# Optimization experiments

Hardware: AMD Instinct MI355X
Metric: run time of the kernel (lower is better)

The kernel has to match this reference:

```python
import jax, jax.numpy as jnp
import numpy as np

N_HEAD = 16


def setup_inputs() -> dict:
    key = jax.random.key(0)
    ks = jax.random.split(key, 6)
    B, S, D = 2, 2048, 1024
    w = 0.02
    return {
        "x": jax.random.normal(ks[0], (B, S, D), dtype=jnp.float32),
        "attention_mask": jnp.ones((B, S), dtype=jnp.int32),
        "Wq": jax.random.normal(ks[1], (D, D), dtype=jnp.float32) * w,
        "bq": jnp.zeros((D,), dtype=jnp.float32),
        "Wk": jax.random.normal(ks[2], (D, D), dtype=jnp.float32) * w,
        "bk": jnp.zeros((D,), dtype=jnp.float32),
        "Wv": jax.random.normal(ks[3], (D, D), dtype=jnp.float32) * w,
        "bv": jnp.zeros((D,), dtype=jnp.float32),
        "Wp": jax.random.normal(ks[4], (D, D), dtype=jnp.float32) * w,
        "bp": jnp.zeros((D,), dtype=jnp.float32),
    }


def reference(x, attention_mask, Wq, bq, Wk, bk, Wv, bv, Wp, bp):
    # x: (B,S,D); PyTorch Linear: y = x @ W.T + b
    B, S, D = x.shape
    H = N_HEAD
    HD = D // H
    scale = 1.0 / jnp.sqrt(jnp.asarray(HD, dtype=x.dtype))

    def heads(W, b):
        return (x @ W.T + b).reshape(B, S, H, HD).transpose(0, 2, 1, 3)  # (B,H,S,HD)

    q = heads(Wq, bq)
    k = heads(Wk, bk)
    v = heads(Wv, bv)

    logits = jnp.einsum("bhsd,bhtd->bhst", q, k) * scale  # (B,H,S,S)

    causal = jnp.tril(jnp.ones((S, S), dtype=bool))  # (S,S)
    am = attention_mask.astype(bool)
    mask = causal[None, None, :, :] & (am[:, None, :, None] & am[:, None, None, :])

    float_min = jnp.finfo(x.dtype).min
    logits = jnp.where(mask, logits, float_min)
    w = jax.nn.softmax(logits, axis=-1)  # dropout is identity in eval / p=0

    attn = jnp.einsum("bhst,bhtd->bhsd", w, v)  # (B,H,S,HD)
    attn = attn.transpose(0, 2, 1, 3).reshape(B, S, D)
    return attn @ Wp.T + bp
```

## Files before the change

### kernel.cpp

```cpp
#include <hip/hip_runtime.h>


#define BB 2
#define SS 2048
#define DD 1024
#define HH 16
#define HDD 64
#define NEG_BIG (-1.0e30f)
#define QSCL 0.18033688011112042f

typedef __attribute__((ext_vector_type(8))) short short8;
typedef __attribute__((ext_vector_type(4))) float floatx4;
typedef unsigned int u32;
#define AS_GLOBAL __attribute__((address_space(1)))
#define AS_LDS    __attribute__((address_space(3)))

__device__ __forceinline__ ushort f2bf(float f) {
    unsigned u = __float_as_uint(f);
    u += 0x7fffu + ((u >> 16) & 1u);
    return (ushort)(u >> 16);
}
__device__ __forceinline__ unsigned pk2(float a, float b) {
    return ((unsigned)f2bf(b) << 16) | (unsigned)f2bf(a);
}
__device__ __forceinline__ unsigned cvtpk(float a, float b) {
    unsigned r;
    asm("v_cvt_pk_bf16_f32 %0, %1, %2" : "=v"(r) : "v"(a), "v"(b));
    return r;
}
__device__ __forceinline__ void unpack8(const uint4 u, float* d) {
    d[0] = __uint_as_float(u.x << 16);
    d[1] = __uint_as_float(u.x & 0xffff0000u);
    d[2] = __uint_as_float(u.y << 16);
    d[3] = __uint_as_float(u.y & 0xffff0000u);
    d[4] = __uint_as_float(u.z << 16);
    d[5] = __uint_as_float(u.z & 0xffff0000u);
    d[6] = __uint_as_float(u.w << 16);
    d[7] = __uint_as_float(u.w & 0xffff0000u);
}
__device__ __forceinline__ void dma16(void* lds, const void* g) {
    __builtin_amdgcn_global_load_lds((const AS_GLOBAL u32*)g, (AS_LDS u32*)lds,
                                     16, 0, 0);
}

__global__ __launch_bounds__(256) void cvt_all(
    const float* __restrict__ x, const float* __restrict__ wq,
    const float* __restrict__ wk, const float* __restrict__ wv,
    const float* __restrict__ wp,
    ushort* __restrict__ dst, ushort* __restrict__ wp_dst)
{
    const size_t flat = ((size_t)blockIdx.x * 256 + threadIdx.x) * 8;
    const float* s;
    ushort* d = dst + flat;
    size_t off;
    float scl = 1.0f;
    if (flat < (size_t)4194304)      { s = x;  off = flat; }
    else if (flat < (size_t)5242880) { s = wq; off = flat - 4194304; scl = QSCL; }
    else if (flat < (size_t)6291456) { s = wk; off = flat - 5242880; }
    else if (flat < (size_t)7340032) { s = wv; off = flat - 6291456; }
    else { s = wp; off = flat - 7340032; d = wp_dst + off; }
    const float4 a = ((const float4*)(s + off))[0];
    const float4 b = ((const float4*)(s + off))[1];
    uint4 u;
    u.x = pk2(a.x * scl, a.y * scl); u.y = pk2(a.z * scl, a.w * scl);
    u.z = pk2(b.x * scl, b.y * scl); u.w = pk2(b.z * scl, b.w * scl);
    *(uint4*)d = u;
}

__global__ __launch_bounds__(256) void gemm_qkv_wa(
    const ushort* __restrict__ A,
    const ushort* __restrict__ W0, const ushort* __restrict__ W1,
    const ushort* __restrict__ W2,
    const float* __restrict__ B0, const float* __restrict__ B1,
    const float* __restrict__ B2,
    ushort* __restrict__ O0, ushort* __restrict__ O1, ushort* __restrict__ O2)
{
    __shared__ ushort As[128 * 32];
    __shared__ ushort Bs[128 * 32];
    __shared__ float bias_s[128];

    const int z = blockIdx.z;
    const ushort* W = (z == 0) ? W0 : (z == 1 ? W1 : W2);
    const float* bias = (z == 0) ? B0 : (z == 1 ? B1 : B2);
    ushort* out = (z == 0) ? O0 : (z == 1 ? O1 : O2);
    const bool isv = (z == 2);

    const int tid = threadIdx.x;
    const int bm = blockIdx.x * 128, bn = blockIdx.y * 128;
    const int wave = tid >> 6, lane = tid & 63, quad = lane >> 4, lm = lane & 15;
    const int r0 = tid >> 2, c0 = (tid & 3) * 8;

    if (tid < 128) {
        float bb = bias[bn + tid];
        if (z == 0) bb *= QSCL;
        bias_s[tid] = bb;
    }

    const floatx4 zz = {0.f, 0.f, 0.f, 0.f};
    floatx4 acc[16];
#pragma unroll
    for (int i = 0; i < 16; ++i) acc[i] = zz;

    for (int k0 = 0; k0 < DD; k0 += 32) {
        __syncthreads();
        dma16(&As[r0 * 32 + c0], A + (size_t)(bm + r0) * DD + k0 + c0);
        dma16(&As[(64 + r0) * 32 + c0], A + (size_t)(bm + 64 + r0) * DD + k0 + c0);
        dma16(&Bs[r0 * 32 + c0], W + (size_t)(bn + r0) * DD + k0 + c0);
        dma16(&Bs[(64 + r0) * 32 + c0], W + (size_t)(bn + 64 + r0) * DD + k0 + c0);
        __syncthreads();

        if (isv) {
            const short8 bf0 = *(const short8*)&Bs[(wave * 32 + lm) * 32 + quad * 8];
            const short8 bf1 = *(const short8*)&Bs[(wave * 32 + 16 + lm) * 32 + quad * 8];
#pragma unroll
            for (int i = 0; i < 8; ++i) {
                const short8 af = *(const short8*)&As[(i * 16 + lm) * 32 + quad * 8];
                acc[i * 2 + 0] = __builtin_amdgcn_mfma_f32_16x16x32_bf16(
                    af, bf0, acc[i * 2 + 0], 0, 0, 0);
                acc[i * 2 + 1] = __builtin_amdgcn_mfma_f32_16x16x32_bf16(
                    af, bf1, acc[i * 2 + 1], 0, 0, 0);
            }
        } else {
            const short8 af0 = *(const short8*)&As[(wave * 32 + lm) * 32 + quad * 8];
            const short8 af1 = *(const short8*)&As[(wave * 32 + 16 + lm) * 32 + quad * 8];
#pragma unroll
            for (int j = 0; j < 8; ++j) {
                const short8 bf = *(const short8*)&Bs[(j * 16 + lm) * 32 + quad * 8];
                acc[j] = __builtin_amdgcn_mfma_f32_16x16x32_bf16(
                    bf, af0, acc[j], 0, 0, 0);
                acc[8 + j] = __builtin_amdgcn_mfma_f32_16x16x32_bf16(
                    bf, af1, acc[8 + j], 0, 0, 0);
            }
        }
    }

    if (isv) {
        const int b = bm >> 11, sbase = bm & 2047;
#pragma unroll
        for (int j = 0; j < 2; ++j) {
            const int n = bn + wave * 32 + j * 16 + lm;
            const float bb = bias_s[n - bn];
            ushort* orow = out + ((size_t)(b * DD + n)) * SS;
#pragma unroll
            for (int i = 0; i < 8; ++i) {
                const floatx4 a = acc[i * 2 + j];
                ushort4 v;
                v.x = f2bf(a[0] + bb); v.y = f2bf(a[1] + bb);
                v.z = f2bf(a[2] + bb); v.w = f2bf(a[3] + bb);
                *(ushort4*)(orow + sbase + i * 16 + quad * 4) = v;
            }
        }
    } else {
#pragma unroll
        for (int i = 0; i < 2; ++i) {
            const int m = bm + wave * 32 + i * 16 + lm;
            const int b = m >> 11, s = m & 2047;
#pragma unroll
            for (int j = 0; j < 8; ++j) {
                const int nl = j * 16 + quad * 4;
                const int n = bn + nl;
                const int h = n >> 6, hd = n & 63;
                const floatx4 a = acc[i * 8 + j];
                ushort4 v;
                v.x = f2bf(a[0] + bias_s[nl + 0]);
                v.y = f2bf(a[1] + bias_s[nl + 1]);
                v.z = f2bf(a[2] + bias_s[nl + 2]);
                v.w = f2bf(a[3] + bias_s[nl + 3]);
                *(ushort4*)(out + (((size_t)(b * HH + h) * SS) + s) * HDD + hd) = v;
            }
        }
    }
}

__global__ __launch_bounds__(256) void gemm_proj_wa(
    const ushort* __restrict__ A, const ushort* __restrict__ W,
    const float* __restrict__ bias, float* __restrict__ out)
{
    __shared__ ushort As[64 * 32];
    __shared__ ushort Bs[128 * 32];
    __shared__ float bias_s[128];

    const int tid = threadIdx.x;
    const int bm = blockIdx.x * 64, bn = blockIdx.y * 128;
    const int wave = tid >> 6, lane = tid & 63, quad = lane >> 4, lm = lane & 15;
    const int r0 = tid >> 2, c0 = (tid & 3) * 8;

    if (tid < 128) bias_s[tid] = bias[bn + tid];

    const floatx4 zz = {0.f, 0.f, 0.f, 0.f};
    floatx4 acc[8];
#pragma unroll
    for (int j = 0; j < 8; ++j) acc[j] = zz;

    for (int k0 = 0; k0 < DD; k0 += 32) {
        __syncthreads();
        dma16(&As[r0 * 32 + c0], A + (size_t)(bm + (r0 & 63)) * DD + k0 + c0);
        dma16(&Bs[r0 * 32 + c0], W + (size_t)(bn + r0) * DD + k0 + c0);
        dma16(&Bs[(64 + r0) * 32 + c0], W + (size_t)(bn + 64 + r0) * DD + k0 + c0);
        __syncthreads();

        const short8 af = *(const short8*)&As[(wave * 16 + lm) * 32 + quad * 8];
#pragma unroll
        for (int j = 0; j < 8; ++j) {
            const short8 bf = *(const short8*)&Bs[(j * 16 + lm) * 32 + quad * 8];
            acc[j] = __builtin_amdgcn_mfma_f32_16x16x32_bf16(bf, af, acc[j], 0, 0, 0);
        }
    }

    const int m = bm + wave * 16 + lm;
#pragma unroll
    for (int j = 0; j < 8; ++j) {
        const int nl = j * 16 + quad * 4;
        float4 v;
        v.x = acc[j][0] + bias_s[nl + 0];
        v.y = acc[j][1] + bias_s[nl + 1];
        v.z = acc[j][2] + bias_s[nl + 2];
        v.w = acc[j][3] + bias_s[nl + 3];
        *(float4*)(out + (size_t)m * DD + bn + nl) = v;
    }
}

__global__ __launch_bounds__(256) void attn_mfma(
    const ushort* __restrict__ Q, const ushort* __restrict__ K,
    const ushort* __restrict__ Vt, const int* __restrict__ am,
    ushort* __restrict__ Opart, float* __restrict__ lbuf)
{
    __shared__ ushort Ks[64 * 72];
    __shared__ ushort Vts[64 * 72];
    __shared__ ushort Ps[4][32 * 72];
    __shared__ int amk_s[64];

    const int tid = threadIdx.x;
    const int wq = tid >> 6, lane = tid & 63, quad = lane >> 4, lm = lane & 15;
    const int bh = blockIdx.y, b = bh >> 4, h = bh & 15;
    const int qt = b ? (int)blockIdx.x : (int)(gridDim.x - 1 - blockIdx.x);
    const int split = blockIdx.z;
    const size_t base = (size_t)bh * SS * HDD;
    const size_t tbase = (size_t)bh * HDD * SS;
    const int* amrow = am + b * SS;
    const int q0 = qt * 128 + wq * 32;

    short8 qf[2][2];
#pragma unroll
    for (int sub = 0; sub < 2; ++sub) {
        const ushort* qp = Q + base + (size_t)(q0 + sub * 16 + lm) * HDD + quad * 8;
        qf[sub][0] = *(const short8*)qp;
        qf[sub][1] = *(const short8*)(qp + 32);
    }
    int amq[2];
#pragma unroll
    for (int sub = 0; sub < 2; ++sub) amq[sub] = amrow[q0 + sub * 16 + lm];
    const bool allq = __all(amq[0] != 0 && amq[1] != 0);

    const floatx4 zz = {0.f, 0.f, 0.f, 0.f};
    floatx4 o_acc[2][4];
#pragma unroll
    for (int sub = 0; sub < 2; ++sub)
#pragma unroll
        for (int n2 = 0; n2 < 4; ++n2) o_acc[sub][n2] = zz;
    float l_lane[2] = {0.f, 0.f};

    const int sr = tid >> 2, sc = (tid & 3) * 16;
    const int ktmax = 2 * qt + 1;

    uint4 kra, krb, vra, vrb;
    int amr = 1;
    {
        const ushort* kp = K + base + (size_t)(split * 64 + sr) * HDD + sc;
        kra = ((const uint4*)kp)[0]; krb = ((const uint4*)kp)[1];
        const ushort* vp = Vt + tbase + (size_t)sr * SS + split * 64 + sc;
        vra = ((const uint4*)vp)[0]; vrb = ((const uint4*)vp)[1];
        if (tid < 64) amr = amrow[split * 64 + tid];
    }
    *(uint4*)&Ks[sr * 72 + sc] = kra;
    *(uint4*)&Ks[sr * 72 + sc + 8] = krb;
    *(uint4*)&Vts[sr * 72 + sc] = vra;
    *(uint4*)&Vts[sr * 72 + sc + 8] = vrb;
    if (tid < 64) amk_s[tid] = amr;
    __syncthreads();

    for (int kt = split; kt <= ktmax; kt += 2) {
        const int nxt = kt + 2;
        const bool have_nxt = nxt <= ktmax;
        if (have_nxt) {
            const ushort* kp = K + base + (size_t)(nxt * 64 + sr) * HDD + sc;
            kra = ((const uint4*)kp)[0]; krb = ((const uint4*)kp)[1];
            const ushort* vp = Vt + tbase + (size_t)sr * SS + nxt * 64 + sc;
            vra = ((const uint4*)vp)[0]; vrb = ((const uint4*)vp)[1];
            if (tid < 64) amr = amrow[nxt * 64 + tid];
        }

        const bool allk = (__ballot(amk_s[lane] != 0) == ~0ull);
        const bool fast = allk & allq & ((kt * 64 + 63) <= q0);
        if (fast) {
#pragma unroll
            for (int nt = 0; nt < 4; ++nt) {
                const short8 kf0 = *(const short8*)&Ks[(nt * 16 + lm) * 72 + quad * 8];
                const short8 kf1 = *(const short8*)&Ks[(nt * 16 + lm) * 72 + 32 + quad * 8];
#pragma unroll
                for (int sub = 0; sub < 2; ++sub) {
                    floatx4 s = zz;
                    s = __builtin_amdgcn_mfma_f32_16x16x32_bf16(kf0, qf[sub][0], s, 0, 0, 0);
                    s = __builtin_amdgcn_mfma_f32_16x16x32_bf16(kf1, qf[sub][1], s, 0, 0, 0);
                    const float e0 = exp2f(fminf(s[0], 40.f));
                    const float e1 = exp2f(fminf(s[1], 40.f));
                    const float e2 = exp2f(fminf(s[2], 40.f));
                    const float e3 = exp2f(fminf(s[3], 40.f));
                    l_lane[sub] += (e0 + e1) + (e2 + e3);
                    uint2 pv;
                    pv.x = cvtpk(e0, e1); pv.y = cvtpk(e2, e3);
                    *(uint2*)&Ps[wq][(sub * 16 + lm) * 72 + nt * 16 + quad * 4] = pv;
                }
            }
        } else {
#pragma unroll
            for (int nt = 0; nt < 4; ++nt) {
                const short8 kf0 = *(const short8*)&Ks[(nt * 16 + lm) * 72 + quad * 8];
                const short8 kf1 = *(const short8*)&Ks[(nt * 16 + lm) * 72 + 32 + quad * 8];
                const int4 amk4 = *(const int4*)&amk_s[nt * 16 + quad * 4];
#pragma unroll
                for (int sub = 0; sub < 2; ++sub) {
                    floatx4 s = zz;
                    s = __builtin_amdgcn_mfma_f32_16x16x32_bf16(kf0, qf[sub][0], s, 0, 0, 0);
                    s = __builtin_amdgcn_mfma_f32_16x16x32_bf16(kf1, qf[sub][1], s, 0, 0, 0);
                    const int qg = q0 + sub * 16 + lm;
                    const int t0 = kt * 64 + nt * 16 + quad * 4;
                    const bool mq = amq[sub] != 0;
                    const bool ok0 = amk4.x && mq && (t0 + 0 <= qg);
                    const bool ok1 = amk4.y && mq && (t0 + 1 <= qg);
                    const bool ok2 = amk4.z && mq && (t0 + 2 <= qg);
                    const bool ok3 = amk4.w && mq && (t0 + 3 <= qg);
                    const float e0 = exp2f(fminf(ok0 ? s[0] : NEG_BIG, 40.f));
                    const float e1 = exp2f(fminf(ok1 ? s[1] : NEG_BIG, 40.f));
                    const float e2 = exp2f(fminf(ok2 ? s[2] : NEG_BIG, 40.f));
                    const float e3 = exp2f(fminf(ok3 ? s[3] : NEG_BIG, 40.f));
                    l_lane[sub] += (e0 + e1) + (e2 + e3);
                    uint2 pv;
                    pv.x = cvtpk(e0, e1); pv.y = cvtpk(e2, e3);
                    *(uint2*)&Ps[wq][(sub * 16 + lm) * 72 + nt * 16 + quad * 4] = pv;
                }
            }
        }

        short8 af[2][2];
#pragma unroll
        for (int sub = 0; sub < 2; ++sub) {
            af[sub][0] = *(const short8*)&Ps[wq][(sub * 16 + lm) * 72 + quad * 8];
            af[sub][1] = *(const short8*)&Ps[wq][(sub * 16 + lm) * 72 + 32 + quad * 8];
        }
#pragma unroll
        for (int n2 = 0; n2 < 4; ++n2) {
            const short8 vf0 = *(const short8*)&Vts[(n2 * 16 + lm) * 72 + quad * 8];
            const short8 vf1 = *(const short8*)&Vts[(n2 * 16 + lm) * 72 + 32 + quad * 8];
#pragma unroll
            for (int sub = 0; sub < 2; ++sub) {
                o_acc[sub][n2] = __builtin_amdgcn_mfma_f32_16x16x32_bf16(
                    vf0, af[sub][0], o_acc[sub][n2], 0, 0, 0);
                o_acc[sub][n2] = __builtin_amdgcn_mfma_f32_16x16x32_bf16(
                    vf1, af[sub][1], o_acc[sub][n2], 0, 0, 0);
            }
        }

        if (have_nxt) {
            __syncthreads();
            *(uint4*)&Ks[sr * 72 + sc] = kra;
            *(uint4*)&Ks[sr * 72 + sc + 8] = krb;
            *(uint4*)&Vts[sr * 72 + sc] = vra;
            *(uint4*)&Vts[sr * 72 + sc + 8] = vrb;
            if (tid < 64) amk_s[tid] = amr;
            __syncthreads();
        }
    }

#pragma unroll
    for (int sub = 0; sub < 2; ++sub) {
        float l = l_lane[sub];
        l += __shfl_xor(l, 16);
        l += __shfl_xor(l, 32);
        if (quad == 0)
            lbuf[(size_t)split * (BB * HH * SS) + (size_t)bh * SS + q0 + sub * 16 + lm] = l;
        const int srow = q0 + sub * 16 + lm;
#pragma unroll
        for (int n2 = 0; n2 < 4; ++n2) {
            uint2 v;
            v.x = cvtpk(o_acc[sub][n2][0], o_acc[sub][n2][1]);
            v.y = cvtpk(o_acc[sub][n2][2], o_acc[sub][n2][3]);
            *(uint2*)(Opart + (size_t)split * (BB * SS * DD)
                        + ((size_t)(b * SS + srow)) * DD + h * HDD + n2 * 16 + quad * 4) = v;
        }
    }
}

__global__ __launch_bounds__(256) void combine(
    const ushort* __restrict__ Opart, const float* __restrict__ lbuf,
    ushort* __restrict__ Aout)
{
    const size_t e = ((size_t)blockIdx.x * 256 + threadIdx.x) * 8;
    const int m = (int)(e >> 10);
    const int col = (int)(e & 1023);
    const int b = m >> 11, s = m & 2047, h = col >> 6;
    const float l = lbuf[(b * HH + h) * SS + s]
                  + lbuf[BB * HH * SS + (b * HH + h) * SS + s];
    const float inv = l > 0.f ? 1.f / l : 0.f;
    const uint4 u0 = *(const uint4*)(Opart + e);
    const uint4 u1 = *(const uint4*)(Opart + (size_t)BB * SS * DD + e);
    float f0[8], f1[8];
    unpack8(u0, f0);
    unpack8(u1, f1);
    uint4 o;
    o.x = pk2((f0[0] + f1[0]) * inv, (f0[1] + f1[1]) * inv);
    o.y = pk2((f0[2] + f1[2]) * inv, (f0[3] + f1[3]) * inv);
    o.z = pk2((f0[4] + f1[4]) * inv, (f0[5] + f1[5]) * inv);
    o.w = pk2((f0[6] + f1[6]) * inv, (f0[7] + f1[7]) * inv);
    *(uint4*)(Aout + e) = o;
}

extern "C" void kernel_launch(void* const* d_in, const int* in_sizes, int n_in,
                              void* d_out, int out_size, void* d_ws, size_t ws_size,
                              hipStream_t stream) {
    const float* x  = (const float*)d_in[0];
    const int*   am = (const int*)d_in[1];
    const float* Wq = (const float*)d_in[2];
    const float* bq = (const float*)d_in[3];
    const float* Wk = (const float*)d_in[4];
    const float* bk = (const float*)d_in[5];
    const float* Wv = (const float*)d_in[6];
    const float* bv = (const float*)d_in[7];
    const float* Wp = (const float*)d_in[8];
    const float* bp = (const float*)d_in[9];
    float* out = (float*)d_out;

    const size_t elems = (size_t)BB * HH * SS * HDD;
    ushort* q_ws = (ushort*)d_ws;
    ushort* k_ws = q_ws + elems;
    ushort* v_ws = k_ws + elems;
    float*  lbuf = (float*)(v_ws + elems);
    ushort* wpb  = (ushort*)(lbuf + 2 * BB * HH * SS);

    ushort* xb  = (ushort*)d_out;
    ushort* wqb = xb + 4194304;
    ushort* wkb = wqb + 1048576;
    ushort* wvb = wkb + 1048576;

    cvt_all<<<4096, 256, 0, stream>>>(x, Wq, Wk, Wv, Wp, xb, wpb);

    gemm_qkv_wa<<<dim3(32, 8, 3), 256, 0, stream>>>(
        xb, wqb, wkb, wvb, bq, bk, bv, q_ws, k_ws, v_ws);

    attn_mfma<<<dim3(SS / 128, BB * HH, 2), 256, 0, stream>>>(
        q_ws, k_ws, v_ws, am, (ushort*)d_out, lbuf);

    combine<<<2048, 256, 0, stream>>>((const ushort*)d_out, lbuf, q_ws);

    gemm_proj_wa<<<dim3(64, 8), 256, 0, stream>>>(q_ws, wpb, bp, out);
}
```

Before: 232.9 us.

## Retile output projection GEMM to 128x128 with register-prefetched K pipeline

```diff
diff --git a/kernel.cpp b/kernel.cpp
--- a/kernel.cpp
+++ b/kernel.cpp
@@ -101,12 +101,20 @@
 #pragma unroll
     for (int i = 0; i < 16; ++i) acc[i] = zz;
 
+    const ushort* a0 = A + (size_t)(bm + r0) * DD + c0;
+    const ushort* a1 = A + (size_t)(bm + 64 + r0) * DD + c0;
+    const ushort* w0 = W + (size_t)(bn + r0) * DD + c0;
+    const ushort* w1 = W + (size_t)(bn + 64 + r0) * DD + c0;
+    ushort* const lA0 = &As[r0 * 32 + c0];
+    ushort* const lA1 = &As[(64 + r0) * 32 + c0];
+    ushort* const lB0 = &Bs[r0 * 32 + c0];
+    ushort* const lB1 = &Bs[(64 + r0) * 32 + c0];
+
     for (int k0 = 0; k0 < DD; k0 += 32) {
         __syncthreads();
-        dma16(&As[r0 * 32 + c0], A + (size_t)(bm + r0) * DD + k0 + c0);
-        dma16(&As[(64 + r0) * 32 + c0], A + (size_t)(bm + 64 + r0) * DD + k0 + c0);
-        dma16(&Bs[r0 * 32 + c0], W + (size_t)(bn + r0) * DD + k0 + c0);
-        dma16(&Bs[(64 + r0) * 32 + c0], W + (size_t)(bn + 64 + r0) * DD + k0 + c0);
+        dma16(lA0, a0); dma16(lA1, a1);
+        dma16(lB0, w0); dma16(lB1, w1);
+        a0 += 32; a1 += 32; w0 += 32; w1 += 32;
         __syncthreads();
 
         if (isv) {
@@ -172,51 +180,93 @@
     }
 }
 
-__global__ __launch_bounds__(256) void gemm_proj_wa(
+__global__ __launch_bounds__(256, 2) void gemm_proj_rs(
     const ushort* __restrict__ A, const ushort* __restrict__ W,
     const float* __restrict__ bias, float* __restrict__ out)
 {
-    __shared__ ushort As[64 * 32];
+    __shared__ ushort As[128 * 32];
     __shared__ ushort Bs[128 * 32];
     __shared__ float bias_s[128];
 
     const int tid = threadIdx.x;
-    const int bm = blockIdx.x * 64, bn = blockIdx.y * 128;
+    const int bm = blockIdx.x * 128, bn = blockIdx.y * 128;
     const int wave = tid >> 6, lane = tid & 63, quad = lane >> 4, lm = lane & 15;
+    const int wm = wave >> 1, wn = wave & 1;
     const int r0 = tid >> 2, c0 = (tid & 3) * 8;
 
     if (tid < 128) bias_s[tid] = bias[bn + tid];
 
     const floatx4 zz = {0.f, 0.f, 0.f, 0.f};
-    floatx4 acc[8];
-#pragma unroll
-    for (int j = 0; j < 8; ++j) acc[j] = zz;
+    floatx4 acc[4][4];
+#pragma unroll
+    for (int i = 0; i < 4; ++i)
+#pragma unroll
+        for (int j = 0; j < 4; ++j) acc[i][j] = zz;
+
+    const ushort* ap = A + (size_t)(bm + r0) * DD + c0;
+    const ushort* wpp = W + (size_t)(bn + r0) * DD + c0;
+
+    uint4 ar0, ar1, wr0, wr1;
+#define LOADT(K0)                                                \
+    do {                                                         \
+        ar0 = *(const uint4*)(ap + (K0));                        \
+        ar1 = *(const uint4*)(ap + (size_t)64 * DD + (K0));      \
+        wr0 = *(const uint4*)(wpp + (K0));                       \
+        wr1 = *(const uint4*)(wpp + (size_t)64 * DD + (K0));     \
+    } while (0)
+#define STORET()                                                 \
+    do {                                                         \
+        *(uint4*)&As[r0 * 32 + c0] = ar0;                        \
+        *(uint4*)&As[(64 + r0) * 32 + c0] = ar1;                 \
+        *(uint4*)&Bs[r0 * 32 + c0] = wr0;                        \
+        *(uint4*)&Bs[(64 + r0) * 32 + c0] = wr1;                 \
+    } while (0)
+
+    LOADT(0);
+    STORET();
+    __syncthreads();
 
     for (int k0 = 0; k0 < DD; k0 += 32) {
-        __syncthreads();
-        dma16(&As[r0 * 32 + c0], A + (size_t)(bm + (r0 & 63)) * DD + k0 + c0);
-        dma16(&Bs[r0 * 32 + c0], W + (size_t)(bn + r0) * DD + k0 + c0);
-        dma16(&Bs[(64 + r0) * 32 + c0], W + (size_t)(bn + 64 + r0) * DD + k0 + c0);
-        __syncthreads();
-
-        const short8 af = *(const short8*)&As[(wave * 16 + lm) * 32 + quad * 8];
-#pragma unroll
-        for (int j = 0; j < 8; ++j) {
-            const short8 bf = *(const short8*)&Bs[(j * 16 + lm) * 32 + quad * 8];
-            acc[j] = __builtin_amdgcn_mfma_f32_16x16x32_bf16(bf, af, acc[j], 0, 0, 0);
-        }
-    }
-
-    const int m = bm + wave * 16 + lm;
-#pragma unroll
-    for (int j = 0; j < 8; ++j) {
-        const int nl = j * 16 + quad * 4;
-        float4 v;
-        v.x = acc[j][0] + bias_s[nl + 0];
-        v.y = acc[j][1] + bias_s[nl + 1];
-        v.z = acc[j][2] + bias_s[nl + 2];
-        v.w = acc[j][3] + bias_s[nl + 3];
-        *(float4*)(out + (size_t)m * DD + bn + nl) = v;
+        const bool have_nxt = (k0 + 32) < DD;
+        if (have_nxt) LOADT(k0 + 32);
+
+        short8 af[4], bf[4];
+#pragma unroll
+        for (int i = 0; i < 4; ++i)
+            af[i] = *(const short8*)&As[(wm * 64 + i * 16 + lm) * 32 + quad * 8];
+#pragma unroll
+        for (int j = 0; j < 4; ++j)
+            bf[j] = *(const short8*)&Bs[(wn * 64 + j * 16 + lm) * 32 + quad * 8];
+#pragma unroll
+        for (int i = 0; i < 4; ++i)
+#pragma unroll
+            for (int j = 0; j < 4; ++j)
+                acc[i][j] = __builtin_amdgcn_mfma_f32_16x16x32_bf16(
+                    bf[j], af[i], acc[i][j], 0, 0, 0);
+
+        if (have_nxt) {
+            __syncthreads();
+            STORET();
+            __syncthreads();
+        }
+    }
+#undef LOADT
+#undef STORET
+
+#pragma unroll
+    for (int i = 0; i < 4; ++i) {
+#pragma unroll
+        for (int j = 0; j < 4; ++j) {
+            const int nl = wn * 64 + j * 16 + quad * 4;
+            const int n = bn + nl;
+            const int m = bm + wm * 64 + i * 16 + lm;
+            float4 v;
+            v.x = acc[i][j][0] + bias_s[nl + 0];
+            v.y = acc[i][j][1] + bias_s[nl + 1];
+            v.z = acc[i][j][2] + bias_s[nl + 2];
+            v.w = acc[i][j][3] + bias_s[nl + 3];
+            *(float4*)(out + (size_t)m * DD + n) = v;
+        }
     }
 }
 
@@ -452,5 +502,5 @@
 
     combine<<<2048, 256, 0, stream>>>((const ushort*)d_out, lbuf, q_ws);
 
-    gemm_proj_wa<<<dim3(64, 8), 256, 0, stream>>>(q_ws, wpb, bp, out);
-}
+    gemm_proj_rs<<<dim3(32, 8), 256, 0, stream>>>(q_ws, wpb, bp, out);
+}
```

Result: faster. 219.7 us (-5.7%).
